# Optimization experiments

Hardware: AMD Instinct MI355X
Metric: run time of the kernel (lower is better)

Reference implementation:

```python
import jax, jax.numpy as jnp
import numpy as np

B, T, I, H, NC = 128, 256, 512, 1024, 1


def setup_inputs() -> dict:
    key = jax.random.key(0)
    ks = jax.random.split(key, 11)
    s = 1.0 / np.sqrt(H)  # torch nn.LSTM default init scale
    return {
        "x": jax.random.normal(ks[0], (B, T, I), jnp.float32),
        "W_ih0": jax.random.normal(ks[1], (4 * H, I), jnp.float32) * s,
        "W_hh0": jax.random.normal(ks[2], (4 * H, H), jnp.float32) * s,
        "b_ih0": jax.random.normal(ks[3], (4 * H,), jnp.float32) * s,
        "b_hh0": jax.random.normal(ks[4], (4 * H,), jnp.float32) * s,
        "W_ih1": jax.random.normal(ks[5], (4 * H, H), jnp.float32) * s,
        "W_hh1": jax.random.normal(ks[6], (4 * H, H), jnp.float32) * s,
        "b_ih1": jax.random.normal(ks[7], (4 * H,), jnp.float32) * s,
        "b_hh1": jax.random.normal(ks[8], (4 * H,), jnp.float32) * s,
        "W_fc": jax.random.normal(ks[9], (NC, H), jnp.float32) * s,
        "b_fc": jax.random.normal(ks[10], (NC,), jnp.float32) * s,
    }


def _lstm_layer(x_seq, W_ih, W_hh, b_ih, b_hh):
    # x_seq: [B, T, F]; torch gate order: i, f, g, o along 4H axis.
    b, h = x_seq.shape[0], W_hh.shape[1]
    # Precompute input projections for all timesteps (one big GEMM).
    x_proj = jnp.einsum("btf,gf->btg", x_seq, W_ih) + b_ih + b_hh  # [B,T,4H]

    def step(carry, xg):
        hprev, cprev = carry
        gates = xg + hprev @ W_hh.T  # [B,4H]
        i, f, g, o = jnp.split(gates, 4, axis=-1)
        c = jax.nn.sigmoid(f) * cprev + jax.nn.sigmoid(i) * jnp.tanh(g)
        hnew = jax.nn.sigmoid(o) * jnp.tanh(c)
        return (hnew, c), hnew

    init = (jnp.zeros((b, h), x_seq.dtype), jnp.zeros((b, h), x_seq.dtype))
    _, hs = jax.lax.scan(step, init, jnp.swapaxes(x_proj, 0, 1))  # [T,B,H]
    return jnp.swapaxes(hs, 0, 1)  # [B,T,H]


def reference(x, W_ih0, W_hh0, b_ih0, b_hh0, W_ih1, W_hh1, b_ih1, b_hh1, W_fc, b_fc):
    h1 = _lstm_layer(x, W_ih0, W_hh0, b_ih0, b_hh0)
    h2 = _lstm_layer(h1, W_ih1, W_hh1, b_ih1, b_hh1)
    return h2[:, -1, :] @ W_fc.T + b_fc  # [B, num_classes]
```

## Files before the change

### kernel.cpp

```cpp
#include <hip/hip_runtime.h>
#include <math.h>

typedef _Float16 half_t;
typedef _Float16 half8 __attribute__((ext_vector_type(8)));
typedef float f32x4 __attribute__((ext_vector_type(4)));
typedef unsigned int u32x4 __attribute__((ext_vector_type(4)));
typedef unsigned long long u64;

#define B_ 128
#define T_ 256
#define I_ 512
#define H_ 1024

#define mfma16 __builtin_amdgcn_mfma_f32_16x16x32_f16

__global__ void k_convert_x(const float* __restrict__ x, half_t* __restrict__ x16, int n8) {
    int i = blockIdx.x * blockDim.x + threadIdx.x;
    if (i >= n8) return;
    const float4* xv = (const float4*)x;
    float4 a = xv[2 * i], b = xv[2 * i + 1];
    half8 o;
    o[0] = (half_t)a.x; o[1] = (half_t)a.y; o[2] = (half_t)a.z; o[3] = (half_t)a.w;
    o[4] = (half_t)b.x; o[5] = (half_t)b.y; o[6] = (half_t)b.z; o[7] = (half_t)b.w;
    int e = i * 8;
    int k = e & (I_ - 1);
    int t = (e >> 9) & (T_ - 1);
    int row = e >> 17;
    ((half8*)x16)[(((size_t)t * B_ + row) * I_ + k) >> 3] = o;
}

__global__ void k_pack_w(const float* __restrict__ Wih, const float* __restrict__ Whh,
                         half_t* __restrict__ out, int Kx, int Ktot) {
    int idx = blockIdx.x * blockDim.x + threadIdx.x;
    int total = 4096 * Ktot;
    if (idx >= total) return;
    int j = idx & 7;
    int lane = (idx >> 3) & 63;
    int nt = (idx >> 9) & 1;
    int rest = idx >> 10;
    int nkb = Ktot >> 5;
    int kb = rest % nkb;
    int hg = rest / nkb;
    int nl = nt * 16 + (lane & 15);
    int gate = nl >> 3, hoff = nl & 7;
    int row = gate * 1024 + hg * 8 + hoff;
    int k = kb * 32 + (lane >> 4) * 8 + j;
    float v = (k < Kx) ? Wih[(size_t)row * Kx + k] : Whh[(size_t)row * 1024 + (k - Kx)];
    out[idx] = (half_t)v;
}

__global__ void k_pack_bias(const float* __restrict__ bih, const float* __restrict__ bhh,
                            float* __restrict__ out) {
    int idx = blockIdx.x * blockDim.x + threadIdx.x;
    if (idx >= 4096) return;
    int hg = idx >> 5, c = idx & 31;
    int gate = c >> 3, hoff = c & 7;
    int row = gate * 1024 + hg * 8 + hoff;
    out[idx] = bih[row] + bhh[row];
}

__global__ void k_zero(unsigned int* __restrict__ p, int n) {
    int i = blockIdx.x * blockDim.x + threadIdx.x;
    if (i < n) p[i] = 0u;
}

__device__ __forceinline__ u64 sysld64(const half_t* p) {
    return __hip_atomic_load((const u64*)p, __ATOMIC_RELAXED, __HIP_MEMORY_SCOPE_SYSTEM);
}
__device__ __forceinline__ void sysst128(half_t* p, half8 v) {
    asm volatile("global_store_dwordx4 %0, %1, off sc0 sc1"
                 :: "v"(p), "v"(v) : "memory");
}
union H8U { half8 h; u64 u[2]; };

#define CHUNK_U32 256
__device__ __forceinline__ void wave_wait(const unsigned* chunk0, unsigned tgt) {
    int lane = threadIdx.x & 63;
    const unsigned* p = chunk0 + (lane & 3) * CHUNK_U32;
    int gd = 0;
    for (;;) {
        u32x4 v; v[0] = tgt; v[1] = tgt; v[2] = tgt; v[3] = tgt;
        if (lane < 4)
            asm volatile("global_load_dwordx4 %0, %1, off sc0 sc1\n\t"
                         "s_waitcnt vmcnt(0)"
                         : "=v"(v) : "v"(p) : "memory");
        if (__all((int)(v[0] >= tgt && v[1] >= tgt && v[2] >= tgt && v[3] >= tgt)))
            break;
        if (gd < 4) __builtin_amdgcn_s_sleep(1);
        else        __builtin_amdgcn_s_sleep(4);
        if (++gd > (1 << 15)) break;
    }
    asm volatile("" ::: "memory");
}

template <int KX, bool LAY1, bool H2SEQ>
__device__ void run_layer(const half_t* __restrict__ srcX,
                          half_t* hA, half_t* hB,
                          const half_t* __restrict__ Wp, const float* __restrict__ biasp,
                          unsigned* flagsPre, unsigned* flagsOwn,
                          int rg, int cg, float* gacc, half_t* hstage)
{
    constexpr int KTOT = KX + 1024;
    constexpr int NKB  = KTOT >> 5;
    constexpr int NI_X = KX >> 8;
    constexpr int NI_H = 4;
    constexpr int NI   = NI_X + NI_H;

    const int tid = threadIdx.x;
    const int ks = tid >> 6, lane = tid & 63;
    const int q = lane >> 4, ml = lane & 15;
    const int hg = cg;
    const int r0 = rg * 32;

    half8 Breg[NI][2];
    {
        const half8* Wp8 = (const half8*)Wp;
        size_t base = (size_t)hg * NKB * 128 + lane;
#pragma unroll
        for (int i = 0; i < NI; ++i) {
            int kb = (i < NI_X) ? (NI_X * ks + i) : (KX / 32 + 4 * ks + (i - NI_X));
            Breg[i][0] = Wp8[base + (size_t)kb * 128];
            Breg[i][1] = Wp8[base + (size_t)kb * 128 + 64];
        }
#pragma unroll
        for (int i = 0; i < NI; ++i)
            asm volatile("" : "+v"(Breg[i][0]), "+v"(Breg[i][1]));
    }

    const int erow = tid >> 3, ehoff = tid & 7;
    float bi = 0.f, bf = 0.f, bgc = 0.f, bo = 0.f;
    if (tid < 256) {
        bi  = biasp[hg * 32 + 0 + ehoff];
        bf  = biasp[hg * 32 + 8 + ehoff];
        bgc = biasp[hg * 32 + 16 + ehoff];
        bo  = biasp[hg * 32 + 24 + ehoff];
    }
    float c_reg = 0.f;

    const unsigned* preC = flagsPre + rg * 8192 + (4 * ks) * CHUNK_U32;
    const unsigned* ownC = flagsOwn + rg * 8192 + (4 * ks) * CHUNK_U32;
    unsigned* myFlag = flagsOwn + rg * 8192 + (cg >> 2) * CHUNK_U32 + (cg & 3);

    for (int t = 0; t < T_; ++t) {
        f32x4 acc[2][2];
        acc[0][0] = (f32x4)0.f; acc[0][1] = (f32x4)0.f;
        acc[1][0] = (f32x4)0.f; acc[1][1] = (f32x4)0.f;

        if constexpr (LAY1) wave_wait(preC, (unsigned)(t + 1));
        const int t1 = LAY1 ? (t + 1) : t;
#pragma unroll
        for (int i = 0; i < NI_X; ++i) {
            int kg = 32 * (NI_X * ks + i) + q * 8;
#pragma unroll
            for (int rt = 0; rt < 2; ++rt) {
                int grow = r0 + rt * 16 + ml;
                half8 a = *(const half8*)(srcX + ((size_t)t1 * B_ + grow) * KX + kg);
                acc[rt][0] = mfma16(a, Breg[i][0], acc[rt][0], 0, 0, 0);
                acc[rt][1] = mfma16(a, Breg[i][1], acc[rt][1], 0, 0, 0);
            }
        }
        if (t > 0) wave_wait(ownC, (unsigned)t);
        const half_t* hp;
        if constexpr (!LAY1 || H2SEQ) hp = hA + (size_t)t * B_ * H_;
        else                          hp = (t & 1) ? hB : hA;
#pragma unroll
        for (int j = 0; j < NI_H; ++j) {
            int i = NI_X + j;
            int kh = 32 * (4 * ks + j) + q * 8;
#pragma unroll
            for (int rt = 0; rt < 2; ++rt) {
                int grow = r0 + rt * 16 + ml;
                half8 a;
                if constexpr (LAY1 && !H2SEQ) {
                    H8U u; const half_t* p = hp + (size_t)grow * H_ + kh;
                    u.u[0] = sysld64(p); u.u[1] = sysld64(p + 4);
                    a = u.h;
                } else {
                    a = *(const half8*)(hp + (size_t)grow * H_ + kh);
                }
                acc[rt][0] = mfma16(a, Breg[i][0], acc[rt][0], 0, 0, 0);
                acc[rt][1] = mfma16(a, Breg[i][1], acc[rt][1], 0, 0, 0);
            }
        }
#pragma unroll
        for (int rt = 0; rt < 2; ++rt)
#pragma unroll
            for (int ct = 0; ct < 2; ++ct)
#pragma unroll
                for (int r = 0; r < 4; ++r) {
                    int rl = rt * 16 + q * 4 + r;
                    int cl = ct * 16 + ml;
                    gacc[(ks * 32 + rl) * 32 + (cl ^ ((rl & 7) << 2))] = acc[rt][ct][r];
                }
        __syncthreads();
        if (tid < 256) {
            int swz = (erow & 7) << 2;
            float pi = 0.f, pf = 0.f, pg = 0.f, po = 0.f;
#pragma unroll
            for (int z = 0; z < 8; ++z) {
                const float* g = &gacc[(z * 32 + erow) * 32];
                pi += g[(0 + ehoff) ^ swz];
                pf += g[(8 + ehoff) ^ swz];
                pg += g[(16 + ehoff) ^ swz];
                po += g[(24 + ehoff) ^ swz];
            }
            pi += bi; pf += bf; pg += bgc; po += bo;
            float si = 1.f / (1.f + __expf(-pi));
            float sf = 1.f / (1.f + __expf(-pf));
            float so = 1.f / (1.f + __expf(-po));
            float tg = 1.f - 2.f / (__expf(2.f * pg) + 1.f);
            c_reg = sf * c_reg + si * tg;
            float th = 1.f - 2.f / (__expf(2.f * c_reg) + 1.f);
            float hn = so * th;
            hstage[erow * 8 + ehoff] = (half_t)hn;
        }
        __syncthreads();
        if (tid < 32) {
            half8 hv = *(const half8*)(hstage + tid * 8);
            half_t* dst;
            if constexpr (!LAY1 || H2SEQ)
                dst = hA + ((size_t)(t + 1) * B_ + (r0 + tid)) * H_ + hg * 8;
            else
                dst = ((t & 1) ? hA : hB) + (size_t)(r0 + tid) * H_ + hg * 8;
            sysst128(dst, hv);
        }
        if (tid == 0) {
            asm volatile("s_waitcnt vmcnt(0)" ::: "memory");
            __hip_atomic_store(myFlag, (unsigned)(t + 1),
                               __ATOMIC_RELAXED, __HIP_MEMORY_SCOPE_SYSTEM);
        }
    }
}

template <bool H2SEQ>
__launch_bounds__(512, 4)
__global__ void lstm_persist(const half_t* __restrict__ x16T, half_t* h1seq,
                             half_t* h2A, half_t* h2B,
                             const half_t* __restrict__ wp0, const half_t* __restrict__ wp1,
                             const float* __restrict__ bias0, const float* __restrict__ bias1,
                             unsigned* __restrict__ flags0, unsigned* __restrict__ flags1)
{
    __shared__ float gacc[8 * 32 * 32];
    __shared__ half_t hstage[32 * 8];
    int bid = blockIdx.x;
    int rg = bid & 3;
    int cg = bid >> 2;

    run_layer<512, false, true>(x16T, h1seq, (half_t*)0, wp0, bias0,
                                flags0, flags0, rg, cg, gacc, hstage);
    run_layer<1024, true, H2SEQ>(h1seq, h2A, h2B, wp1, bias1,
                                 flags0, flags1, rg, cg, gacc, hstage);
}

__global__ void k_fc(const half_t* __restrict__ h, const float* __restrict__ Wfc,
                     const float* __restrict__ bfc, float* __restrict__ out) {
    int m = blockIdx.x, lane = threadIdx.x;
    float s = 0.f;
    for (int k = lane; k < H_; k += 64) s += (float)h[m * H_ + k] * Wfc[k];
#pragma unroll
    for (int o = 32; o; o >>= 1) s += __shfl_down(s, o, 64);
    if (lane == 0) out[m] = s + bfc[0];
}

extern "C" void kernel_launch(void* const* d_in, const int* in_sizes, int n_in,
                              void* d_out, int out_size, void* d_ws, size_t ws_size,
                              hipStream_t stream) {
    const float* x    = (const float*)d_in[0];
    const float* Wih0 = (const float*)d_in[1];
    const float* Whh0 = (const float*)d_in[2];
    const float* bih0 = (const float*)d_in[3];
    const float* bhh0 = (const float*)d_in[4];
    const float* Wih1 = (const float*)d_in[5];
    const float* Whh1 = (const float*)d_in[6];
    const float* bih1 = (const float*)d_in[7];
    const float* bhh1 = (const float*)d_in[8];
    const float* Wfc  = (const float*)d_in[9];
    const float* bfc  = (const float*)d_in[10];
    float* out = (float*)d_out;

    char* ws = (char*)d_ws;
    size_t off = 0;
    auto carve = [&](size_t bytes) { void* p = ws + off; off += (bytes + 255) & ~(size_t)255; return p; };
    half_t* x16T   = (half_t*)carve((size_t)B_ * T_ * I_ * 2);
    half_t* h1seq  = (half_t*)carve((size_t)(T_ + 1) * B_ * H_ * 2);
    half_t* wp0    = (half_t*)carve((size_t)4096 * 1536 * 2);
    half_t* wp1    = (half_t*)carve((size_t)4096 * 2048 * 2);
    float*  bias0  = (float*)carve(4096 * 4);
    float*  bias1  = (float*)carve(4096 * 4);
    char*   states = (char*)carve(2 * (size_t)B_ * H_ * 2 + 262144 + 256);
    if (off > ws_size) return;

    half_t* h2a = (half_t*)states;
    half_t* h2b = h2a + B_ * H_;
    unsigned* flags0 = (unsigned*)(h2b + B_ * H_);
    unsigned* flags1 = flags0 + 4 * 8192;

    half_t* h2seq = nullptr;
    if (off + (size_t)(T_ + 1) * B_ * H_ * 2 + 256 <= ws_size)
        h2seq = (half_t*)carve((size_t)(T_ + 1) * B_ * H_ * 2);

    k_convert_x<<<(B_ * T_ * I_ / 8 + 255) / 256, 256, 0, stream>>>(x, x16T, B_ * T_ * I_ / 8);
    k_pack_w<<<(4096 * 1536 + 255) / 256, 256, 0, stream>>>(Wih0, Whh0, wp0, 512, 1536);
    k_pack_w<<<(4096 * 2048 + 255) / 256, 256, 0, stream>>>(Wih1, Whh1, wp1, 1024, 2048);
    k_pack_bias<<<16, 256, 0, stream>>>(bih0, bhh0, bias0);
    k_pack_bias<<<16, 256, 0, stream>>>(bih1, bhh1, bias1);
    k_zero<<<(B_ * H_ / 2 + 255) / 256, 256, 0, stream>>>((unsigned int*)h1seq, B_ * H_ / 2);
    {
        int n = (2 * B_ * H_ * 2 + 262144 + 256) / 4;
        k_zero<<<(n + 255) / 256, 256, 0, stream>>>((unsigned int*)states, n);
    }
    if (h2seq)
        k_zero<<<(B_ * H_ / 2 + 255) / 256, 256, 0, stream>>>((unsigned int*)h2seq, B_ * H_ / 2);

    if (h2seq) {
        lstm_persist<true><<<dim3(512), dim3(512), 0, stream>>>(
            x16T, h1seq, h2seq, (half_t*)0, wp0, wp1, bias0, bias1, flags0, flags1);
        k_fc<<<128, 64, 0, stream>>>(h2seq + (size_t)T_ * B_ * H_, Wfc, bfc, out);
    } else {
        lstm_persist<false><<<dim3(512), dim3(512), 0, stream>>>(
            x16T, h1seq, h2a, h2b, wp0, wp1, bias0, bias1, flags0, flags1);
        k_fc<<<128, 64, 0, stream>>>(h2a, Wfc, bfc, out);
    }
}
```

Baseline: 4.594 ms.

## Wavefront-pipeline both LSTM layers in one persistent block with split waves

Replaces the two sequential layer passes with a wavefront schedule. Each 1024-thread block runs layer 0 at step e in its first 8 waves and layer 1 at step e-1 in the other 8, so the two recurrences overlap instead of running back to back. Rows per block grow from 32 to 64 over 256 blocks, flags are shrunk and polled by one wave per block followed by a block barrier, and h2 always uses the full sequence buffer. The cost is heavier register pressure at 1024 threads with 4 blocks per CU requested, plus extra block-wide barriers per step.

```diff
diff --git a/kernel.cpp b/kernel.cpp
--- a/kernel.cpp
+++ b/kernel.cpp
@@ -64,192 +64,249 @@
     if (i < n) p[i] = 0u;
 }
 
-__device__ __forceinline__ u64 sysld64(const half_t* p) {
-    return __hip_atomic_load((const u64*)p, __ATOMIC_RELAXED, __HIP_MEMORY_SCOPE_SYSTEM);
-}
 __device__ __forceinline__ void sysst128(half_t* p, half8 v) {
     asm volatile("global_store_dwordx4 %0, %1, off sc0 sc1"
                  :: "v"(p), "v"(v) : "memory");
 }
-union H8U { half8 h; u64 u[2]; };
-
-#define CHUNK_U32 256
-__device__ __forceinline__ void wave_wait(const unsigned* chunk0, unsigned tgt) {
-    int lane = threadIdx.x & 63;
-    const unsigned* p = chunk0 + (lane & 3) * CHUNK_U32;
-    int gd = 0;
-    for (;;) {
-        u32x4 v; v[0] = tgt; v[1] = tgt; v[2] = tgt; v[3] = tgt;
-        if (lane < 4)
-            asm volatile("global_load_dwordx4 %0, %1, off sc0 sc1\n\t"
-                         "s_waitcnt vmcnt(0)"
-                         : "=v"(v) : "v"(p) : "memory");
-        if (__all((int)(v[0] >= tgt && v[1] >= tgt && v[2] >= tgt && v[3] >= tgt)))
-            break;
-        if (gd < 4) __builtin_amdgcn_s_sleep(1);
-        else        __builtin_amdgcn_s_sleep(4);
-        if (++gd > (1 << 15)) break;
-    }
-    asm volatile("" ::: "memory");
-}
-
-template <int KX, bool LAY1, bool H2SEQ>
-__device__ void run_layer(const half_t* __restrict__ srcX,
-                          half_t* hA, half_t* hB,
-                          const half_t* __restrict__ Wp, const float* __restrict__ biasp,
-                          unsigned* flagsPre, unsigned* flagsOwn,
-                          int rg, int cg, float* gacc, half_t* hstage)
+
+__launch_bounds__(1024, 4)
+__global__ void lstm_persist(const half_t* __restrict__ x16T,
+                             half_t* h1seq, half_t* h2seq,
+                             const half_t* __restrict__ wp0, const half_t* __restrict__ wp1,
+                             const float* __restrict__ bias0, const float* __restrict__ bias1,
+                             unsigned* __restrict__ flags)
 {
-    constexpr int KTOT = KX + 1024;
-    constexpr int NKB  = KTOT >> 5;
-    constexpr int NI_X = KX >> 8;
-    constexpr int NI_H = 4;
-    constexpr int NI   = NI_X + NI_H;
-
+    __shared__ float gacc[2 * 8 * 32 * 32];
+    __shared__ half_t hstg[2][512];
+    const int bid = blockIdx.x;
+    const int rgB = bid & 1;
+    const int cg  = bid >> 1;
+    const int hg  = cg;
+    const int r0  = rgB * 64;
     const int tid = threadIdx.x;
-    const int ks = tid >> 6, lane = tid & 63;
+    const int w   = tid >> 6;
+    const int lane = tid & 63;
     const int q = lane >> 4, ml = lane & 15;
-    const int hg = cg;
-    const int r0 = rg * 32;
-
-    half8 Breg[NI][2];
-    {
-        const half8* Wp8 = (const half8*)Wp;
-        size_t base = (size_t)hg * NKB * 128 + lane;
-#pragma unroll
-        for (int i = 0; i < NI; ++i) {
-            int kb = (i < NI_X) ? (NI_X * ks + i) : (KX / 32 + 4 * ks + (i - NI_X));
-            Breg[i][0] = Wp8[base + (size_t)kb * 128];
-            Breg[i][1] = Wp8[base + (size_t)kb * 128 + 64];
+    unsigned* fl = flags + rgB * 512;
+
+    if (w < 8) {
+        const int ks = w;
+        half8 B0[6][2];
+        {
+            const half8* W = (const half8*)wp0;
+            size_t base = (size_t)hg * 48 * 128 + lane;
+#pragma unroll
+            for (int i = 0; i < 6; ++i) {
+                int kb = (i < 2) ? (2 * ks + i) : (16 + 4 * ks + (i - 2));
+                B0[i][0] = W[base + (size_t)kb * 128];
+                B0[i][1] = W[base + (size_t)kb * 128 + 64];
+            }
+#pragma unroll
+            for (int i = 0; i < 6; ++i)
+                asm volatile("" : "+v"(B0[i][0]), "+v"(B0[i][1]));
         }
-#pragma unroll
-        for (int i = 0; i < NI; ++i)
-            asm volatile("" : "+v"(Breg[i][0]), "+v"(Breg[i][1]));
-    }
-
-    const int erow = tid >> 3, ehoff = tid & 7;
-    float bi = 0.f, bf = 0.f, bgc = 0.f, bo = 0.f;
-    if (tid < 256) {
-        bi  = biasp[hg * 32 + 0 + ehoff];
-        bf  = biasp[hg * 32 + 8 + ehoff];
-        bgc = biasp[hg * 32 + 16 + ehoff];
-        bo  = biasp[hg * 32 + 24 + ehoff];
-    }
-    float c_reg = 0.f;
-
-    const unsigned* preC = flagsPre + rg * 8192 + (4 * ks) * CHUNK_U32;
-    const unsigned* ownC = flagsOwn + rg * 8192 + (4 * ks) * CHUNK_U32;
-    unsigned* myFlag = flagsOwn + rg * 8192 + (cg >> 2) * CHUNK_U32 + (cg & 3);
-
-    for (int t = 0; t < T_; ++t) {
-        f32x4 acc[2][2];
-        acc[0][0] = (f32x4)0.f; acc[0][1] = (f32x4)0.f;
-        acc[1][0] = (f32x4)0.f; acc[1][1] = (f32x4)0.f;
-
-        if constexpr (LAY1) wave_wait(preC, (unsigned)(t + 1));
-        const int t1 = LAY1 ? (t + 1) : t;
-#pragma unroll
-        for (int i = 0; i < NI_X; ++i) {
-            int kg = 32 * (NI_X * ks + i) + q * 8;
-#pragma unroll
-            for (int rt = 0; rt < 2; ++rt) {
-                int grow = r0 + rt * 16 + ml;
-                half8 a = *(const half8*)(srcX + ((size_t)t1 * B_ + grow) * KX + kg);
-                acc[rt][0] = mfma16(a, Breg[i][0], acc[rt][0], 0, 0, 0);
-                acc[rt][1] = mfma16(a, Breg[i][1], acc[rt][1], 0, 0, 0);
+        const int lay = tid >> 8;
+        const int idx = tid & 255;
+        const int row = idx >> 3, hoff = idx & 7;
+        const float* bp = lay ? bias1 : bias0;
+        const float bi = bp[hg * 32 + hoff],      bf = bp[hg * 32 + 8 + hoff];
+        const float bg = bp[hg * 32 + 16 + hoff], bo = bp[hg * 32 + 24 + hoff];
+        float cA = 0.f, cB = 0.f;
+        unsigned* myF0 = fl + cg;
+        unsigned* myF1 = fl + 128 + cg;
+
+        for (int e = 0; e <= T_; ++e) {
+            if (e > 0) {
+                if (tid < 64) {
+                    unsigned tgt = (lane < 32) ? (unsigned)e : (unsigned)(e - 1);
+                    const unsigned* p = (lane < 32) ? (fl + lane * 4)
+                                                    : (fl + 128 + (lane - 32) * 4);
+                    int gd = 0;
+                    for (;;) {
+                        u32x4 v;
+                        asm volatile("global_load_dwordx4 %0, %1, off sc0 sc1\n\t"
+                                     "s_waitcnt vmcnt(0)"
+                                     : "=v"(v) : "v"(p) : "memory");
+                        if (__all((int)(v[0] >= tgt && v[1] >= tgt &&
+                                        v[2] >= tgt && v[3] >= tgt))) break;
+                        __builtin_amdgcn_s_sleep(2);
+                        if (++gd > (1 << 15)) break;
+                    }
+                }
+                __syncthreads();
+                asm volatile("" ::: "memory");
+            }
+            f32x4 acc[4][2];
+            if (e < T_) {
+#pragma unroll
+                for (int rt = 0; rt < 4; ++rt) { acc[rt][0] = (f32x4)0.f; acc[rt][1] = (f32x4)0.f; }
+#pragma unroll
+                for (int i = 0; i < 6; ++i) {
+                    int kb = (i < 2) ? (2 * ks + i) : (16 + 4 * ks + (i - 2));
+                    int kg = kb * 32 + q * 8;
+#pragma unroll
+                    for (int rt = 0; rt < 4; ++rt) {
+                        int grow = r0 + rt * 16 + ml;
+                        const half_t* ap = (i < 2)
+                            ? x16T + ((size_t)e * B_ + grow) * I_ + kg
+                            : h1seq + ((size_t)e * B_ + grow) * H_ + (kg - I_);
+                        half8 a = *(const half8*)ap;
+                        acc[rt][0] = mfma16(a, B0[i][0], acc[rt][0], 0, 0, 0);
+                        acc[rt][1] = mfma16(a, B0[i][1], acc[rt][1], 0, 0, 0);
+                    }
+                }
+#pragma unroll
+                for (int rt = 0; rt < 2; ++rt)
+#pragma unroll
+                    for (int ct = 0; ct < 2; ++ct)
+#pragma unroll
+                        for (int r = 0; r < 4; ++r) {
+                            int rl = rt * 16 + q * 4 + r;
+                            int cl = ct * 16 + ml;
+                            gacc[ks * 1024 + rl * 32 + (cl ^ ((rl & 7) << 2))] = acc[rt][ct][r];
+                        }
+            }
+            __syncthreads();
+            bool valid = (lay == 0) ? (e < T_) : (e >= 1);
+            if (tid < 512 && valid) {
+                const float* gb = gacc + lay * 8192;
+                int swz = (row & 7) << 2;
+                float pi = 0.f, pf = 0.f, pg = 0.f, po = 0.f;
+#pragma unroll
+                for (int z = 0; z < 8; ++z) {
+                    const float* g = gb + z * 1024 + row * 32;
+                    pi += g[(0 + hoff) ^ swz];
+                    pf += g[(8 + hoff) ^ swz];
+                    pg += g[(16 + hoff) ^ swz];
+                    po += g[(24 + hoff) ^ swz];
+                }
+                pi += bi; pf += bf; pg += bg; po += bo;
+                float si = 1.f / (1.f + __expf(-pi));
+                float sf = 1.f / (1.f + __expf(-pf));
+                float so = 1.f / (1.f + __expf(-po));
+                float tg = 1.f - 2.f / (__expf(2.f * pg) + 1.f);
+                cA = sf * cA + si * tg;
+                float th = 1.f - 2.f / (__expf(2.f * cA) + 1.f);
+                hstg[lay][row * 8 + hoff] = (half_t)(so * th);
+            }
+            __syncthreads();
+            if (e < T_) {
+#pragma unroll
+                for (int rt = 2; rt < 4; ++rt)
+#pragma unroll
+                    for (int ct = 0; ct < 2; ++ct)
+#pragma unroll
+                        for (int r = 0; r < 4; ++r) {
+                            int rl = (rt - 2) * 16 + q * 4 + r;
+                            int cl = ct * 16 + ml;
+                            gacc[ks * 1024 + rl * 32 + (cl ^ ((rl & 7) << 2))] = acc[rt][ct][r];
+                        }
+            }
+            __syncthreads();
+            if (tid < 512 && valid) {
+                const float* gb = gacc + lay * 8192;
+                int swz = (row & 7) << 2;
+                float pi = 0.f, pf = 0.f, pg = 0.f, po = 0.f;
+#pragma unroll
+                for (int z = 0; z < 8; ++z) {
+                    const float* g = gb + z * 1024 + row * 32;
+                    pi += g[(0 + hoff) ^ swz];
+                    pf += g[(8 + hoff) ^ swz];
+                    pg += g[(16 + hoff) ^ swz];
+                    po += g[(24 + hoff) ^ swz];
+                }
+                pi += bi; pf += bf; pg += bg; po += bo;
+                float si = 1.f / (1.f + __expf(-pi));
+                float sf = 1.f / (1.f + __expf(-pf));
+                float so = 1.f / (1.f + __expf(-po));
+                float tg = 1.f - 2.f / (__expf(2.f * pg) + 1.f);
+                cB = sf * cB + si * tg;
+                float th = 1.f - 2.f / (__expf(2.f * cB) + 1.f);
+                hstg[lay][(row + 32) * 8 + hoff] = (half_t)(so * th);
+            }
+            __syncthreads();
+            if (tid < 64) {
+                if (e < T_)
+                    sysst128(h1seq + ((size_t)(e + 1) * B_ + r0 + lane) * H_ + hg * 8,
+                             *(const half8*)&hstg[0][lane * 8]);
+                if (e >= 1)
+                    sysst128(h2seq + ((size_t)e * B_ + r0 + lane) * H_ + hg * 8,
+                             *(const half8*)&hstg[1][lane * 8]);
+            }
+            if (tid == 0) {
+                asm volatile("s_waitcnt vmcnt(0)" ::: "memory");
+                if (e < T_) __hip_atomic_store(myF0, (unsigned)(e + 1),
+                                               __ATOMIC_RELAXED, __HIP_MEMORY_SCOPE_SYSTEM);
+                if (e >= 1) __hip_atomic_store(myF1, (unsigned)e,
+                                               __ATOMIC_RELAXED, __HIP_MEMORY_SCOPE_SYSTEM);
             }
         }
-        if (t > 0) wave_wait(ownC, (unsigned)t);
-        const half_t* hp;
-        if constexpr (!LAY1 || H2SEQ) hp = hA + (size_t)t * B_ * H_;
-        else                          hp = (t & 1) ? hB : hA;
-#pragma unroll
-        for (int j = 0; j < NI_H; ++j) {
-            int i = NI_X + j;
-            int kh = 32 * (4 * ks + j) + q * 8;
-#pragma unroll
-            for (int rt = 0; rt < 2; ++rt) {
-                int grow = r0 + rt * 16 + ml;
-                half8 a;
-                if constexpr (LAY1 && !H2SEQ) {
-                    H8U u; const half_t* p = hp + (size_t)grow * H_ + kh;
-                    u.u[0] = sysld64(p); u.u[1] = sysld64(p + 4);
-                    a = u.h;
-                } else {
-                    a = *(const half8*)(hp + (size_t)grow * H_ + kh);
-                }
-                acc[rt][0] = mfma16(a, Breg[i][0], acc[rt][0], 0, 0, 0);
-                acc[rt][1] = mfma16(a, Breg[i][1], acc[rt][1], 0, 0, 0);
-            }
+    } else {
+        const int ks = w - 8;
+        half8 B1[8][2];
+        {
+            const half8* W = (const half8*)wp1;
+            size_t base = (size_t)hg * 64 * 128 + lane;
+#pragma unroll
+            for (int i = 0; i < 8; ++i) {
+                int kb = (i < 4) ? (4 * ks + i) : (32 + 4 * ks + (i - 4));
+                B1[i][0] = W[base + (size_t)kb * 128];
+                B1[i][1] = W[base + (size_t)kb * 128 + 64];
+            }
+#pragma unroll
+            for (int i = 0; i < 8; ++i)
+                asm volatile("" : "+v"(B1[i][0]), "+v"(B1[i][1]));
         }
-#pragma unroll
-        for (int rt = 0; rt < 2; ++rt)
-#pragma unroll
-            for (int ct = 0; ct < 2; ++ct)
-#pragma unroll
-                for (int r = 0; r < 4; ++r) {
-                    int rl = rt * 16 + q * 4 + r;
-                    int cl = ct * 16 + ml;
-                    gacc[(ks * 32 + rl) * 32 + (cl ^ ((rl & 7) << 2))] = acc[rt][ct][r];
-                }
-        __syncthreads();
-        if (tid < 256) {
-            int swz = (erow & 7) << 2;
-            float pi = 0.f, pf = 0.f, pg = 0.f, po = 0.f;
-#pragma unroll
-            for (int z = 0; z < 8; ++z) {
-                const float* g = &gacc[(z * 32 + erow) * 32];
-                pi += g[(0 + ehoff) ^ swz];
-                pf += g[(8 + ehoff) ^ swz];
-                pg += g[(16 + ehoff) ^ swz];
-                po += g[(24 + ehoff) ^ swz];
-            }
-            pi += bi; pf += bf; pg += bgc; po += bo;
-            float si = 1.f / (1.f + __expf(-pi));
-            float sf = 1.f / (1.f + __expf(-pf));
-            float so = 1.f / (1.f + __expf(-po));
-            float tg = 1.f - 2.f / (__expf(2.f * pg) + 1.f);
-            c_reg = sf * c_reg + si * tg;
-            float th = 1.f - 2.f / (__expf(2.f * c_reg) + 1.f);
-            float hn = so * th;
-            hstage[erow * 8 + ehoff] = (half_t)hn;
-        }
-        __syncthreads();
-        if (tid < 32) {
-            half8 hv = *(const half8*)(hstage + tid * 8);
-            half_t* dst;
-            if constexpr (!LAY1 || H2SEQ)
-                dst = hA + ((size_t)(t + 1) * B_ + (r0 + tid)) * H_ + hg * 8;
-            else
-                dst = ((t & 1) ? hA : hB) + (size_t)(r0 + tid) * H_ + hg * 8;
-            sysst128(dst, hv);
-        }
-        if (tid == 0) {
-            asm volatile("s_waitcnt vmcnt(0)" ::: "memory");
-            __hip_atomic_store(myFlag, (unsigned)(t + 1),
-                               __ATOMIC_RELAXED, __HIP_MEMORY_SCOPE_SYSTEM);
+        for (int e = 0; e <= T_; ++e) {
+            if (e > 0) { __syncthreads(); asm volatile("" ::: "memory"); }
+            f32x4 acc[4][2];
+            if (e >= 1) {
+#pragma unroll
+                for (int rt = 0; rt < 4; ++rt) { acc[rt][0] = (f32x4)0.f; acc[rt][1] = (f32x4)0.f; }
+#pragma unroll
+                for (int i = 0; i < 8; ++i) {
+                    int kb = (i < 4) ? (4 * ks + i) : (32 + 4 * ks + (i - 4));
+                    int ko = kb * 32 + q * 8;
+#pragma unroll
+                    for (int rt = 0; rt < 4; ++rt) {
+                        int grow = r0 + rt * 16 + ml;
+                        const half_t* ap = (i < 4)
+                            ? h1seq + ((size_t)e * B_ + grow) * H_ + ko
+                            : h2seq + ((size_t)(e - 1) * B_ + grow) * H_ + (ko - 1024);
+                        half8 a = *(const half8*)ap;
+                        acc[rt][0] = mfma16(a, B1[i][0], acc[rt][0], 0, 0, 0);
+                        acc[rt][1] = mfma16(a, B1[i][1], acc[rt][1], 0, 0, 0);
+                    }
+                }
+#pragma unroll
+                for (int rt = 0; rt < 2; ++rt)
+#pragma unroll
+                    for (int ct = 0; ct < 2; ++ct)
+#pragma unroll
+                        for (int r = 0; r < 4; ++r) {
+                            int rl = rt * 16 + q * 4 + r;
+                            int cl = ct * 16 + ml;
+                            gacc[8192 + ks * 1024 + rl * 32 + (cl ^ ((rl & 7) << 2))] = acc[rt][ct][r];
+                        }
+            }
+            __syncthreads();
+            __syncthreads();
+            if (e >= 1) {
+#pragma unroll
+                for (int rt = 2; rt < 4; ++rt)
+#pragma unroll
+                    for (int ct = 0; ct < 2; ++ct)
+#pragma unroll
+                        for (int r = 0; r < 4; ++r) {
+                            int rl = (rt - 2) * 16 + q * 4 + r;
+                            int cl = ct * 16 + ml;
+                            gacc[8192 + ks * 1024 + rl * 32 + (cl ^ ((rl & 7) << 2))] = acc[rt][ct][r];
+                        }
+            }
+            __syncthreads();
+            __syncthreads();
         }
     }
-}
-
-template <bool H2SEQ>
-__launch_bounds__(512, 4)
-__global__ void lstm_persist(const half_t* __restrict__ x16T, half_t* h1seq,
-                             half_t* h2A, half_t* h2B,
-                             const half_t* __restrict__ wp0, const half_t* __restrict__ wp1,
-                             const float* __restrict__ bias0, const float* __restrict__ bias1,
-                             unsigned* __restrict__ flags0, unsigned* __restrict__ flags1)
-{
-    __shared__ float gacc[8 * 32 * 32];
-    __shared__ half_t hstage[32 * 8];
-    int bid = blockIdx.x;
-    int rg = bid & 3;
-    int cg = bid >> 2;
-
-    run_layer<512, false, true>(x16T, h1seq, (half_t*)0, wp0, bias0,
-                                flags0, flags0, rg, cg, gacc, hstage);
-    run_layer<1024, true, H2SEQ>(h1seq, h2A, h2B, wp1, bias1,
-                                 flags0, flags1, rg, cg, gacc, hstage);
 }
 
 __global__ void k_fc(const half_t* __restrict__ h, const float* __restrict__ Wfc,
@@ -283,21 +340,13 @@
     auto carve = [&](size_t bytes) { void* p = ws + off; off += (bytes + 255) & ~(size_t)255; return p; };
     half_t* x16T   = (half_t*)carve((size_t)B_ * T_ * I_ * 2);
     half_t* h1seq  = (half_t*)carve((size_t)(T_ + 1) * B_ * H_ * 2);
+    half_t* h2seq  = (half_t*)carve((size_t)(T_ + 1) * B_ * H_ * 2);
     half_t* wp0    = (half_t*)carve((size_t)4096 * 1536 * 2);
     half_t* wp1    = (half_t*)carve((size_t)4096 * 2048 * 2);
     float*  bias0  = (float*)carve(4096 * 4);
     float*  bias1  = (float*)carve(4096 * 4);
-    char*   states = (char*)carve(2 * (size_t)B_ * H_ * 2 + 262144 + 256);
+    unsigned* flags = (unsigned*)carve(1024 * 4);
     if (off > ws_size) return;
-
-    half_t* h2a = (half_t*)states;
-    half_t* h2b = h2a + B_ * H_;
-    unsigned* flags0 = (unsigned*)(h2b + B_ * H_);
-    unsigned* flags1 = flags0 + 4 * 8192;
-
-    half_t* h2seq = nullptr;
-    if (off + (size_t)(T_ + 1) * B_ * H_ * 2 + 256 <= ws_size)
-        h2seq = (half_t*)carve((size_t)(T_ + 1) * B_ * H_ * 2);
 
     k_convert_x<<<(B_ * T_ * I_ / 8 + 255) / 256, 256, 0, stream>>>(x, x16T, B_ * T_ * I_ / 8);
     k_pack_w<<<(4096 * 1536 + 255) / 256, 256, 0, stream>>>(Wih0, Whh0, wp0, 512, 1536);
@@ -305,20 +354,11 @@
     k_pack_bias<<<16, 256, 0, stream>>>(bih0, bhh0, bias0);
     k_pack_bias<<<16, 256, 0, stream>>>(bih1, bhh1, bias1);
     k_zero<<<(B_ * H_ / 2 + 255) / 256, 256, 0, stream>>>((unsigned int*)h1seq, B_ * H_ / 2);
-    {
-        int n = (2 * B_ * H_ * 2 + 262144 + 256) / 4;
-        k_zero<<<(n + 255) / 256, 256, 0, stream>>>((unsigned int*)states, n);
-    }
-    if (h2seq)
-        k_zero<<<(B_ * H_ / 2 + 255) / 256, 256, 0, stream>>>((unsigned int*)h2seq, B_ * H_ / 2);
-
-    if (h2seq) {
-        lstm_persist<true><<<dim3(512), dim3(512), 0, stream>>>(
-            x16T, h1seq, h2seq, (half_t*)0, wp0, wp1, bias0, bias1, flags0, flags1);
-        k_fc<<<128, 64, 0, stream>>>(h2seq + (size_t)T_ * B_ * H_, Wfc, bfc, out);
-    } else {
-        lstm_persist<false><<<dim3(512), dim3(512), 0, stream>>>(
-            x16T, h1seq, h2a, h2b, wp0, wp1, bias0, bias1, flags0, flags1);
-        k_fc<<<128, 64, 0, stream>>>(h2a, Wfc, bfc, out);
-    }
-}
+    k_zero<<<(B_ * H_ / 2 + 255) / 256, 256, 0, stream>>>((unsigned int*)h2seq, B_ * H_ / 2);
+    k_zero<<<4, 256, 0, stream>>>(flags, 1024);
+
+    lstm_persist<<<dim3(256), dim3(1024), 0, stream>>>(
+        x16T, h1seq, h2seq, wp0, wp1, bias0, bias1, flags);
+
+    k_fc<<<128, 64, 0, stream>>>(h2seq + (size_t)T_ * B_ * H_, Wfc, bfc, out);
+}
```

After: 6.082 ms. +32.4%, slower.
